# Kernel tuning notes

Hardware: AMD Instinct MI355X
Metric: run time of the kernel (lower is better)

Reference implementation:

```python
import jax, jax.numpy as jnp
import numpy as np

NUM_EMB = 1024
EMB_DIM = 256
BETA = 0.25


def setup_inputs() -> dict:
    key = jax.random.key(0)
    k1, k2 = jax.random.split(key)
    z_e = jax.random.normal(k1, (32, EMB_DIM, 32, 32), dtype=jnp.float32)
    # original inits uniform(-1/num_emb, 1/num_emb)
    emb_weight = jax.random.uniform(k2, (NUM_EMB, EMB_DIM), dtype=jnp.float32,
                                    minval=-1.0 / NUM_EMB, maxval=1.0 / NUM_EMB)
    return {"z_e": z_e, "emb_weight": emb_weight}


def reference(z_e, emb_weight):
    # (B, C, H, W) -> (B, H, W, C)
    z = jnp.transpose(z_e, (0, 2, 3, 1))
    B, H, W, C = z.shape
    z_flat = z.reshape(-1, C)  # (N, C)
    # squared L2 distances to codebook: ||z||^2 + ||e||^2 - 2 z e^T
    d = (jnp.sum(z_flat ** 2, axis=1, keepdims=True)
         + jnp.sum(emb_weight ** 2, axis=1)
         - 2.0 * jnp.matmul(z_flat, emb_weight.T))  # (N, num_emb)
    encoding_indices = jnp.argmin(d, axis=1)  # (N,)
    # one-hot matmul == gather of codebook rows
    z_q = jnp.take(emb_weight, encoding_indices, axis=0).reshape(B, H, W, C)
    # vq losses
    L_e = jnp.mean((jax.lax.stop_gradient(z_q) - z) ** 2)
    L_q = jnp.mean((z_q - jax.lax.stop_gradient(z)) ** 2)
    vq_loss = L_e + BETA * L_q
    # straight-through estimator
    z_q_st = z + jax.lax.stop_gradient(z_q - z)
    z_q_out = jnp.transpose(z_q_st, (0, 3, 1, 2))  # (B, C, H, W)
    return z_q_out, vq_loss, encoding_indices
```

## Files before the change

kernel.cpp:

```cpp
#include <hip/hip_runtime.h>

#define NUM_EMB 1024
#define EMB_DIM 256
#define NPIX    32768
#define HW      1024
#define ZQ_ELEMS 8388608

#define WS_TNORM 8
#define WS_SNORM 8192
#define WS_KEYS  139264
#define WS_EPL   401408
#define EPLANE_ELEMS (NUM_EMB * EMB_DIM)

typedef unsigned long long u64;
typedef unsigned int u32;
typedef unsigned short u16;

typedef __bf16 bf16x8 __attribute__((ext_vector_type(8)));
typedef float f32x4 __attribute__((ext_vector_type(4)));
typedef u16 u16x8 __attribute__((ext_vector_type(8)));

__device__ __forceinline__ float pw128_sq(const float* x, int stride) {
  float r[8];
#pragma unroll
  for (int j = 0; j < 8; ++j) {
    float v = x[(size_t)j * stride];
    r[j] = __fmul_rn(v, v);
  }
  for (int i = 8; i < 128; i += 8) {
#pragma unroll
    for (int j = 0; j < 8; ++j) {
      float v = x[(size_t)(i + j) * stride];
      r[j] = __fadd_rn(r[j], __fmul_rn(v, v));
    }
  }
  float s01 = __fadd_rn(r[0], r[1]);
  float s23 = __fadd_rn(r[2], r[3]);
  float s45 = __fadd_rn(r[4], r[5]);
  float s67 = __fadd_rn(r[6], r[7]);
  return __fadd_rn(__fadd_rn(s01, s23), __fadd_rn(s45, s67));
}

__device__ __forceinline__ void split3(float x, u16& h, u16& m, u16& l) {
  u32 u = __float_as_uint(x);
  u16 hb = (u16)((u + 0x7fffu + ((u >> 16) & 1u)) >> 16);
  float hf = __uint_as_float((u32)hb << 16);
  float r1 = x - hf;
  u32 u1 = __float_as_uint(r1);
  u16 mb = (u16)((u1 + 0x7fffu + ((u1 >> 16) & 1u)) >> 16);
  float mf = __uint_as_float((u32)mb << 16);
  float r2 = r1 - mf;
  u32 u2 = __float_as_uint(r2);
  u16 lb = (u16)((u2 + 0x7fffu + ((u2 >> 16) & 1u)) >> 16);
  h = hb; m = mb; l = lb;
}

__device__ __forceinline__ u64 shfl_xor_u64(u64 v, int msk) {
  const u32 lo = __shfl_xor((u32)v, msk, 64);
  const u32 hi = __shfl_xor((u32)(v >> 32), msk, 64);
  return ((u64)hi << 32) | lo;
}

__global__ __launch_bounds__(256) void vq_prep_kernel(
    const float* __restrict__ z, const float* __restrict__ emb,
    float* __restrict__ tnorm, float* __restrict__ snorm,
    unsigned long long* __restrict__ keys, double* __restrict__ loss_accum,
    u16* __restrict__ eh, u16* __restrict__ em, u16* __restrict__ el) {
  const int gid = blockIdx.x * 256 + threadIdx.x;
  if (gid == 0) *loss_accum = 0.0;
  if (gid < NPIX) {
    keys[gid] = ~0ull;
    const int b = gid >> 10, hw = gid & 1023;
    const float* base = z + (size_t)b * (EMB_DIM * HW) + hw;
    snorm[gid] = __fadd_rn(pw128_sq(base, HW), pw128_sq(base + (size_t)128 * HW, HW));
  } else {
    const int k = gid - NPIX;
    if (k < NUM_EMB) {
      const float* row = emb + (size_t)k * EMB_DIM;
      tnorm[k] = __fadd_rn(pw128_sq(row, 1), pw128_sq(row + 128, 1));
      for (int c = 0; c < EMB_DIM; c += 8) {
        u16x8 vh, vm, vl;
#pragma unroll
        for (int j = 0; j < 8; ++j) {
          u16 h_, m_, l_;
          split3(row[c + j], h_, m_, l_);
          vh[j] = h_; vm[j] = m_; vl[j] = l_;
        }
        *(u16x8*)(eh + (size_t)k * EMB_DIM + c) = vh;
        *(u16x8*)(em + (size_t)k * EMB_DIM + c) = vm;
        *(u16x8*)(el + (size_t)k * EMB_DIM + c) = vl;
      }
    }
  }
}

__global__ __launch_bounds__(256, 2) void vq_main_kernel(
    const float* __restrict__ z,
    const u16* __restrict__ eh, const u16* __restrict__ em,
    const u16* __restrict__ el,
    const float* __restrict__ tnorm, const float* __restrict__ snorm,
    unsigned long long* __restrict__ keys) {
  __shared__ __align__(16) u16 zs[3][128][40];
  __shared__ __align__(16) u16 es[3][128][40];

  const int t   = threadIdx.x;
  const int hb  = blockIdx.x;
  const int bid = (hb & 7) * 256 + (hb >> 3);
  const int pt  = bid >> 3;
  const int ntb = bid & 7;
  const int m0  = pt * 128;
  const int n0  = ntb * 128;
  const int b   = m0 >> 10;
  const int hw0 = m0 & 1023;
  const float* zbase = z + (size_t)b * (EMB_DIM * HW) + hw0;

  const int l    = t & 63;
  const int wid  = t >> 6;
  const int wpx0 = (wid >> 1) * 64;
  const int wcb  = (wid & 1) * 64;

  const int za  = (t & 15) + ((t >> 6) << 4);
  const int p0  = za * 2;
  const int kq  = (t >> 4) & 3;
  const int ecode = t >> 1;
  const int ekh   = (t & 1) * 16;
  const u16* eplanes[3] = {eh, em, el};
  const size_t ebase = (size_t)(n0 + ecode) * EMB_DIM + ekh;

  float2 gz[8];
  u16x8  ge[3][2];

#pragma unroll
  for (int j = 0; j < 8; ++j)
    gz[j] = *(const float2*)(zbase + (size_t)(kq * 8 + j) * HW + p0);
#pragma unroll
  for (int p = 0; p < 3; ++p) {
    const u16* src = eplanes[p] + ebase;
    ge[p][0] = *(const u16x8*)(src);
    ge[p][1] = *(const u16x8*)(src + 8);
  }

  f32x4 acc[4][4];
#pragma unroll
  for (int i = 0; i < 4; ++i)
#pragma unroll
    for (int j = 0; j < 4; ++j) {
      f32x4 zv = {0.0f, 0.0f, 0.0f, 0.0f};
      acc[i][j] = zv;
    }

  for (int kt = 0; kt < 8; ++kt) {
#pragma unroll
    for (int r = 0; r < 2; ++r) {
      u16x8 vh, vm, vl;
#pragma unroll
      for (int j = 0; j < 8; ++j) {
        const float x = r ? gz[j].y : gz[j].x;
        u16 h_, m_, l_;
        split3(x, h_, m_, l_);
        vh[j] = h_; vm[j] = m_; vl[j] = l_;
      }
      *(u16x8*)&zs[0][p0 + r][kq * 8] = vh;
      *(u16x8*)&zs[1][p0 + r][kq * 8] = vm;
      *(u16x8*)&zs[2][p0 + r][kq * 8] = vl;
    }
#pragma unroll
    for (int p = 0; p < 3; ++p) {
      *(u16x8*)&es[p][ecode][ekh]     = ge[p][0];
      *(u16x8*)&es[p][ecode][ekh + 8] = ge[p][1];
    }

    if (kt < 7) {
      const int kb = (kt + 1) * 32;
#pragma unroll
      for (int j = 0; j < 8; ++j)
        gz[j] = *(const float2*)(zbase + (size_t)(kb + kq * 8 + j) * HW + p0);
#pragma unroll
      for (int p = 0; p < 3; ++p) {
        const u16* src = eplanes[p] + ebase + kb;
        ge[p][0] = *(const u16x8*)(src);
        ge[p][1] = *(const u16x8*)(src + 8);
      }
    }
    __syncthreads();

    const int frow = l & 15;
    const int kg8  = (l >> 4) * 8;
    bf16x8 af[3][4], bf[3][4];
#pragma unroll
    for (int mt = 0; mt < 4; ++mt)
#pragma unroll
      for (int p = 0; p < 3; ++p)
        af[p][mt] = *(const bf16x8*)&zs[p][wpx0 + mt * 16 + frow][kg8];
#pragma unroll
    for (int nn = 0; nn < 4; ++nn)
#pragma unroll
      for (int p = 0; p < 3; ++p)
        bf[p][nn] = *(const bf16x8*)&es[p][wcb + nn * 16 + frow][kg8];

#define MMPAIR(PA, PB)                                                        \
    _Pragma("unroll")                                                         \
    for (int mt = 0; mt < 4; ++mt) {                                          \
      _Pragma("unroll")                                                       \
      for (int nn = 0; nn < 4; ++nn)                                          \
        acc[mt][nn] = __builtin_amdgcn_mfma_f32_16x16x32_bf16(                \
            af[PA][mt], bf[PB][nn], acc[mt][nn], 0, 0, 0);                    \
    }
    MMPAIR(0, 0)
    MMPAIR(0, 1)
    MMPAIR(1, 0)
    MMPAIR(1, 1)
    MMPAIR(0, 2)
    MMPAIR(2, 0)
#undef MMPAIR
    __syncthreads();
  }

  float sv[4][4], tv[4];
#pragma unroll
  for (int mt = 0; mt < 4; ++mt)
#pragma unroll
    for (int r = 0; r < 4; ++r)
      sv[mt][r] = snorm[m0 + wpx0 + mt * 16 + (l >> 4) * 4 + r];
#pragma unroll
  for (int nn = 0; nn < 4; ++nn)
    tv[nn] = tnorm[n0 + wcb + nn * 16 + (l & 15)];

  u64 bk[4][4];
#pragma unroll
  for (int mt = 0; mt < 4; ++mt)
#pragma unroll
    for (int r = 0; r < 4; ++r) {
      u64 best = ~0ull;
#pragma unroll
      for (int nn = 0; nn < 4; ++nn) {
        const float d =
            __fsub_rn(__fadd_rn(sv[mt][r], tv[nn]), 2.0f * acc[mt][nn][r]);
        const u64 key = ((u64)__float_as_uint(d) << 32) |
                        (u32)(n0 + wcb + nn * 16 + (l & 15));
        best = key < best ? key : best;
      }
      bk[mt][r] = best;
    }
#pragma unroll
  for (int off = 1; off < 16; off <<= 1) {
#pragma unroll
    for (int mt = 0; mt < 4; ++mt)
#pragma unroll
      for (int r = 0; r < 4; ++r) {
        const u64 o = shfl_xor_u64(bk[mt][r], off);
        if (o < bk[mt][r]) bk[mt][r] = o;
      }
  }

  u64* part = (u64*)&zs[0][0][0];
  if ((l & 15) == 0) {
#pragma unroll
    for (int mt = 0; mt < 4; ++mt)
#pragma unroll
      for (int r = 0; r < 4; ++r)
        part[(wpx0 + mt * 16 + (l >> 4) * 4 + r) * 2 + (wid & 1)] = bk[mt][r];
  }
  __syncthreads();
  if (t < 128) {
    const u64 a = part[t * 2], c = part[t * 2 + 1];
    atomicMin(&keys[m0 + t], a < c ? a : c);
  }
}

__global__ __launch_bounds__(256) void vq_outputs_kernel(
    const float* __restrict__ z, const float* __restrict__ emb,
    const unsigned long long* __restrict__ keys, float* __restrict__ out,
    float* __restrict__ out_idx_f, double* __restrict__ loss_accum) {
  const int t  = threadIdx.x;
  const int n0 = blockIdx.x * 64;
  const int m  = t & 63;
  const int c0 = t >> 6;
  const int b  = n0 >> 10;
  const int hw = n0 & 1023;
  const float* zb = z   + (size_t)b * (EMB_DIM * HW) + hw + m;
  float*       ob = out + (size_t)b * (EMB_DIM * HW) + hw + m;
  const int idx = (int)(u32)(keys[n0 + m] & 0xffffffffu);
  const float* er = emb + (size_t)idx * EMB_DIM;
  if (c0 == 0) out_idx_f[n0 + m] = (float)idx;

  double lsum = 0.0;
  for (int c = c0; c < EMB_DIM; c += 4) {
    const float e  = er[c];
    const float zv = zb[(size_t)c * HW];
    const float diff = e - zv;
    const float zq   = zv + diff;
    ob[(size_t)c * HW] = zq;
    lsum += (double)diff * (double)diff;
  }

  __shared__ double red[256];
  red[t] = lsum;
  __syncthreads();
  for (int s2 = 128; s2 > 0; s2 >>= 1) {
    if (t < s2) red[t] += red[t + s2];
    __syncthreads();
  }
  if (t == 0) atomicAdd(loss_accum, red[0]);
}

__global__ void vq_finalize_kernel(const double* __restrict__ loss_accum,
                                   float* __restrict__ out_loss) {
  const float L = (float)(*loss_accum / (double)ZQ_ELEMS);
  out_loss[0] = __fadd_rn(L, __fmul_rn(0.25f, L));
}

extern "C" void kernel_launch(void* const* d_in, const int* in_sizes, int n_in,
                              void* d_out, int out_size, void* d_ws, size_t ws_size,
                              hipStream_t stream) {
  const float* z   = (const float*)d_in[0];
  const float* emb = (const float*)d_in[1];

  float* out       = (float*)d_out;
  float* out_loss  = out + ZQ_ELEMS;
  float* out_idx_f = out + ZQ_ELEMS + 1;

  double* loss_accum = (double*)d_ws;
  float*  tnorm = (float*)((char*)d_ws + WS_TNORM);
  float*  snorm = (float*)((char*)d_ws + WS_SNORM);
  unsigned long long* keys = (unsigned long long*)((char*)d_ws + WS_KEYS);
  u16* eh = (u16*)((char*)d_ws + WS_EPL);
  u16* em = eh + EPLANE_ELEMS;
  u16* el = em + EPLANE_ELEMS;

  vq_prep_kernel<<<132, 256, 0, stream>>>(z, emb, tnorm, snorm, keys, loss_accum,
                                          eh, em, el);
  vq_main_kernel<<<2048, 256, 0, stream>>>(z, eh, em, el, tnorm, snorm, keys);
  vq_outputs_kernel<<<NPIX / 64, 256, 0, stream>>>(z, emb, keys, out, out_idx_f,
                                                   loss_accum);
  vq_finalize_kernel<<<1, 1, 0, stream>>>(loss_accum, out_loss);
}
```

Before: 179.9 us.

## Use 32x32 MFMA with direct-to-register codebook loads and fuse loss finalize

The main kernel switches from 16x16x32 to 32x32x16 bf16 MFMA tiles. Codebook split-plane fragments now load straight from global memory into registers, dropping the shared-memory staging buffer for them. The z staging layout changes to scalar loads per pixel. The separate finalize kernel is folded into the outputs kernel through a last-block atomic counter, saving one launch. In exchange the codebook loads sit uncoalesced on the critical path with no prefetch, and the epilogue reads snorm per register.

New measurement: 217.5 us. 20.9% more time.

```diff
diff --git a/kernel.cpp b/kernel.cpp
--- a/kernel.cpp
+++ b/kernel.cpp
@@ -9,7 +9,8 @@
 #define WS_TNORM 8
 #define WS_SNORM 8192
 #define WS_KEYS  139264
-#define WS_EPL   401408
+#define WS_CNT   401408
+#define WS_EPL   401424
 #define EPLANE_ELEMS (NUM_EMB * EMB_DIM)
 
 typedef unsigned long long u64;
@@ -17,7 +18,7 @@
 typedef unsigned short u16;
 
 typedef __bf16 bf16x8 __attribute__((ext_vector_type(8)));
-typedef float f32x4 __attribute__((ext_vector_type(4)));
+typedef float f32x16 __attribute__((ext_vector_type(16)));
 typedef u16 u16x8 __attribute__((ext_vector_type(8)));
 
 __device__ __forceinline__ float pw128_sq(const float* x, int stride) {
@@ -65,9 +66,11 @@
     const float* __restrict__ z, const float* __restrict__ emb,
     float* __restrict__ tnorm, float* __restrict__ snorm,
     unsigned long long* __restrict__ keys, double* __restrict__ loss_accum,
+    u32* __restrict__ counter,
     u16* __restrict__ eh, u16* __restrict__ em, u16* __restrict__ el) {
   const int gid = blockIdx.x * 256 + threadIdx.x;
   if (gid == 0) *loss_accum = 0.0;
+  if (gid == 1) *counter = 0u;
   if (gid < NPIX) {
     keys[gid] = ~0ull;
     const int b = gid >> 10, hw = gid & 1023;
@@ -101,7 +104,6 @@
     const float* __restrict__ tnorm, const float* __restrict__ snorm,
     unsigned long long* __restrict__ keys) {
   __shared__ __align__(16) u16 zs[3][128][40];
-  __shared__ __align__(16) u16 es[3][128][40];
 
   const int t   = threadIdx.x;
   const int hb  = blockIdx.x;
@@ -118,148 +120,125 @@
   const int wid  = t >> 6;
   const int wpx0 = (wid >> 1) * 64;
   const int wcb  = (wid & 1) * 64;
-
-  const int za  = (t & 15) + ((t >> 6) << 4);
-  const int p0  = za * 2;
-  const int kq  = (t >> 4) & 3;
-  const int ecode = t >> 1;
-  const int ekh   = (t & 1) * 16;
-  const u16* eplanes[3] = {eh, em, el};
-  const size_t ebase = (size_t)(n0 + ecode) * EMB_DIM + ekh;
-
-  float2 gz[8];
-  u16x8  ge[3][2];
-
-#pragma unroll
-  for (int j = 0; j < 8; ++j)
-    gz[j] = *(const float2*)(zbase + (size_t)(kq * 8 + j) * HW + p0);
-#pragma unroll
-  for (int p = 0; p < 3; ++p) {
-    const u16* src = eplanes[p] + ebase;
-    ge[p][0] = *(const u16x8*)(src);
-    ge[p][1] = *(const u16x8*)(src + 8);
-  }
-
-  f32x4 acc[4][4];
-#pragma unroll
-  for (int i = 0; i < 4; ++i)
-#pragma unroll
-    for (int j = 0; j < 4; ++j) {
-      f32x4 zv = {0.0f, 0.0f, 0.0f, 0.0f};
-      acc[i][j] = zv;
-    }
+  const int cl   = l & 31;
+  const int hi   = l >> 5;
+
+  const int spx = t & 127;
+  const int skh = (t >> 7) * 16;
+
+  const u16* eplan[3] = {eh, em, el};
+  size_t ebase[2];
+  ebase[0] = (size_t)(n0 + wcb + cl) * EMB_DIM + (size_t)hi * 8;
+  ebase[1] = (size_t)(n0 + wcb + 32 + cl) * EMB_DIM + (size_t)hi * 8;
+
+  float gz[16];
+#pragma unroll
+  for (int j = 0; j < 16; ++j)
+    gz[j] = zbase[(size_t)(skh + j) * HW + spx];
+
+  f32x16 acc[2][2];
+#pragma unroll
+  for (int i = 0; i < 2; ++i)
+#pragma unroll
+    for (int j = 0; j < 2; ++j)
+#pragma unroll
+      for (int r = 0; r < 16; ++r) acc[i][j][r] = 0.0f;
 
   for (int kt = 0; kt < 8; ++kt) {
 #pragma unroll
-    for (int r = 0; r < 2; ++r) {
+    for (int c = 0; c < 2; ++c) {
       u16x8 vh, vm, vl;
 #pragma unroll
       for (int j = 0; j < 8; ++j) {
-        const float x = r ? gz[j].y : gz[j].x;
         u16 h_, m_, l_;
-        split3(x, h_, m_, l_);
+        split3(gz[c * 8 + j], h_, m_, l_);
         vh[j] = h_; vm[j] = m_; vl[j] = l_;
       }
-      *(u16x8*)&zs[0][p0 + r][kq * 8] = vh;
-      *(u16x8*)&zs[1][p0 + r][kq * 8] = vm;
-      *(u16x8*)&zs[2][p0 + r][kq * 8] = vl;
-    }
-#pragma unroll
-    for (int p = 0; p < 3; ++p) {
-      *(u16x8*)&es[p][ecode][ekh]     = ge[p][0];
-      *(u16x8*)&es[p][ecode][ekh + 8] = ge[p][1];
-    }
-
+      *(u16x8*)&zs[0][spx][skh + c * 8] = vh;
+      *(u16x8*)&zs[1][spx][skh + c * 8] = vm;
+      *(u16x8*)&zs[2][spx][skh + c * 8] = vl;
+    }
     if (kt < 7) {
       const int kb = (kt + 1) * 32;
 #pragma unroll
-      for (int j = 0; j < 8; ++j)
-        gz[j] = *(const float2*)(zbase + (size_t)(kb + kq * 8 + j) * HW + p0);
-#pragma unroll
-      for (int p = 0; p < 3; ++p) {
-        const u16* src = eplanes[p] + ebase + kb;
-        ge[p][0] = *(const u16x8*)(src);
-        ge[p][1] = *(const u16x8*)(src + 8);
-      }
-    }
+      for (int j = 0; j < 16; ++j)
+        gz[j] = zbase[(size_t)(kb + skh + j) * HW + spx];
+    }
+    bf16x8 ge[3][2][2];
+#pragma unroll
+    for (int p = 0; p < 3; ++p)
+#pragma unroll
+      for (int nn = 0; nn < 2; ++nn)
+#pragma unroll
+        for (int ks = 0; ks < 2; ++ks)
+          ge[p][nn][ks] =
+              *(const bf16x8*)(eplan[p] + ebase[nn] + (size_t)kt * 32 + ks * 16);
     __syncthreads();
 
-    const int frow = l & 15;
-    const int kg8  = (l >> 4) * 8;
-    bf16x8 af[3][4], bf[3][4];
-#pragma unroll
-    for (int mt = 0; mt < 4; ++mt)
+#pragma unroll
+    for (int ks = 0; ks < 2; ++ks) {
+      bf16x8 af[3][2];
 #pragma unroll
       for (int p = 0; p < 3; ++p)
-        af[p][mt] = *(const bf16x8*)&zs[p][wpx0 + mt * 16 + frow][kg8];
-#pragma unroll
-    for (int nn = 0; nn < 4; ++nn)
-#pragma unroll
-      for (int p = 0; p < 3; ++p)
-        bf[p][nn] = *(const bf16x8*)&es[p][wcb + nn * 16 + frow][kg8];
-
-#define MMPAIR(PA, PB)                                                        \
-    _Pragma("unroll")                                                         \
-    for (int mt = 0; mt < 4; ++mt) {                                          \
+#pragma unroll
+        for (int mt = 0; mt < 2; ++mt)
+          af[p][mt] =
+              *(const bf16x8*)&zs[p][wpx0 + mt * 32 + cl][ks * 16 + hi * 8];
+#define PROD(PA, PB)                                                          \
       _Pragma("unroll")                                                       \
-      for (int nn = 0; nn < 4; ++nn)                                          \
-        acc[mt][nn] = __builtin_amdgcn_mfma_f32_16x16x32_bf16(                \
-            af[PA][mt], bf[PB][nn], acc[mt][nn], 0, 0, 0);                    \
-    }
-    MMPAIR(0, 0)
-    MMPAIR(0, 1)
-    MMPAIR(1, 0)
-    MMPAIR(1, 1)
-    MMPAIR(0, 2)
-    MMPAIR(2, 0)
-#undef MMPAIR
+      for (int mt = 0; mt < 2; ++mt) {                                        \
+        _Pragma("unroll")                                                     \
+        for (int nn = 0; nn < 2; ++nn)                                        \
+          acc[mt][nn] = __builtin_amdgcn_mfma_f32_32x32x16_bf16(              \
+              af[PA][mt], ge[PB][nn][ks], acc[mt][nn], 0, 0, 0);              \
+      }
+      PROD(0, 0)
+      PROD(0, 1)
+      PROD(1, 0)
+      PROD(1, 1)
+      PROD(0, 2)
+      PROD(2, 0)
+#undef PROD
+    }
     __syncthreads();
   }
 
-  float sv[4][4], tv[4];
-#pragma unroll
-  for (int mt = 0; mt < 4; ++mt)
-#pragma unroll
-    for (int r = 0; r < 4; ++r)
-      sv[mt][r] = snorm[m0 + wpx0 + mt * 16 + (l >> 4) * 4 + r];
-#pragma unroll
-  for (int nn = 0; nn < 4; ++nn)
-    tv[nn] = tnorm[n0 + wcb + nn * 16 + (l & 15)];
-
-  u64 bk[4][4];
-#pragma unroll
-  for (int mt = 0; mt < 4; ++mt)
-#pragma unroll
-    for (int r = 0; r < 4; ++r) {
-      u64 best = ~0ull;
-#pragma unroll
-      for (int nn = 0; nn < 4; ++nn) {
-        const float d =
-            __fsub_rn(__fadd_rn(sv[mt][r], tv[nn]), 2.0f * acc[mt][nn][r]);
-        const u64 key = ((u64)__float_as_uint(d) << 32) |
-                        (u32)(n0 + wcb + nn * 16 + (l & 15));
-        best = key < best ? key : best;
-      }
-      bk[mt][r] = best;
-    }
-#pragma unroll
-  for (int off = 1; off < 16; off <<= 1) {
-#pragma unroll
-    for (int mt = 0; mt < 4; ++mt)
-#pragma unroll
-      for (int r = 0; r < 4; ++r) {
-        const u64 o = shfl_xor_u64(bk[mt][r], off);
-        if (o < bk[mt][r]) bk[mt][r] = o;
+  const float tv0 = tnorm[n0 + wcb + cl];
+  const float tv1 = tnorm[n0 + wcb + 32 + cl];
+  u64 bk[2][16];
+#pragma unroll
+  for (int mt = 0; mt < 2; ++mt)
+#pragma unroll
+    for (int reg = 0; reg < 16; ++reg) {
+      const int row = wpx0 + mt * 32 + (reg & 3) + 8 * (reg >> 2) + 4 * hi;
+      const float s = snorm[m0 + row];
+      const float d0 = __fsub_rn(__fadd_rn(s, tv0), 2.0f * acc[mt][0][reg]);
+      const float d1 = __fsub_rn(__fadd_rn(s, tv1), 2.0f * acc[mt][1][reg]);
+      const u64 k0 = ((u64)__float_as_uint(d0) << 32) | (u32)(n0 + wcb + cl);
+      const u64 k1 =
+          ((u64)__float_as_uint(d1) << 32) | (u32)(n0 + wcb + 32 + cl);
+      bk[mt][reg] = k0 < k1 ? k0 : k1;
+    }
+#pragma unroll
+  for (int off = 1; off < 32; off <<= 1) {
+#pragma unroll
+    for (int mt = 0; mt < 2; ++mt)
+#pragma unroll
+      for (int reg = 0; reg < 16; ++reg) {
+        const u64 o = shfl_xor_u64(bk[mt][reg], off);
+        if (o < bk[mt][reg]) bk[mt][reg] = o;
       }
   }
 
   u64* part = (u64*)&zs[0][0][0];
-  if ((l & 15) == 0) {
-#pragma unroll
-    for (int mt = 0; mt < 4; ++mt)
-#pragma unroll
-      for (int r = 0; r < 4; ++r)
-        part[(wpx0 + mt * 16 + (l >> 4) * 4 + r) * 2 + (wid & 1)] = bk[mt][r];
+  if (cl == 0) {
+#pragma unroll
+    for (int mt = 0; mt < 2; ++mt)
+#pragma unroll
+      for (int reg = 0; reg < 16; ++reg) {
+        const int row = wpx0 + mt * 32 + (reg & 3) + 8 * (reg >> 2) + 4 * hi;
+        part[row * 2 + (wid & 1)] = bk[mt][reg];
+      }
   }
   __syncthreads();
   if (t < 128) {
@@ -271,7 +250,8 @@
 __global__ __launch_bounds__(256) void vq_outputs_kernel(
     const float* __restrict__ z, const float* __restrict__ emb,
     const unsigned long long* __restrict__ keys, float* __restrict__ out,
-    float* __restrict__ out_idx_f, double* __restrict__ loss_accum) {
+    float* __restrict__ out_idx_f, double* __restrict__ loss_accum,
+    u32* __restrict__ counter, float* __restrict__ out_loss) {
   const int t  = threadIdx.x;
   const int n0 = blockIdx.x * 64;
   const int m  = t & 63;
@@ -301,13 +281,16 @@
     if (t < s2) red[t] += red[t + s2];
     __syncthreads();
   }
-  if (t == 0) atomicAdd(loss_accum, red[0]);
-}
-
-__global__ void vq_finalize_kernel(const double* __restrict__ loss_accum,
-                                   float* __restrict__ out_loss) {
-  const float L = (float)(*loss_accum / (double)ZQ_ELEMS);
-  out_loss[0] = __fadd_rn(L, __fmul_rn(0.25f, L));
+  if (t == 0) {
+    atomicAdd(loss_accum, red[0]);
+    __threadfence();
+    const u32 tick = atomicAdd(counter, 1u);
+    if (tick == (u32)(NPIX / 64 - 1)) {
+      const double total = atomicAdd(loss_accum, 0.0);
+      const float L = (float)(total / (double)ZQ_ELEMS);
+      out_loss[0] = __fadd_rn(L, __fmul_rn(0.25f, L));
+    }
+  }
 }
 
 extern "C" void kernel_launch(void* const* d_in, const int* in_sizes, int n_in,
@@ -324,14 +307,14 @@
   float*  tnorm = (float*)((char*)d_ws + WS_TNORM);
   float*  snorm = (float*)((char*)d_ws + WS_SNORM);
   unsigned long long* keys = (unsigned long long*)((char*)d_ws + WS_KEYS);
+  u32* counter = (u32*)((char*)d_ws + WS_CNT);
   u16* eh = (u16*)((char*)d_ws + WS_EPL);
   u16* em = eh + EPLANE_ELEMS;
   u16* el = em + EPLANE_ELEMS;
 
   vq_prep_kernel<<<132, 256, 0, stream>>>(z, emb, tnorm, snorm, keys, loss_accum,
-                                          eh, em, el);
+                                          counter, eh, em, el);
   vq_main_kernel<<<2048, 256, 0, stream>>>(z, eh, em, el, tnorm, snorm, keys);
   vq_outputs_kernel<<<NPIX / 64, 256, 0, stream>>>(z, emb, keys, out, out_idx_f,
-                                                   loss_accum);
-  vq_finalize_kernel<<<1, 1, 0, stream>>>(loss_accum, out_loss);
-}
+                                                   loss_accum, counter, out_loss);
+}
```
